# Kernel optimization log

Hardware: AMD Instinct MI355X
Metric: run time of the kernel (lower is better)

The kernel has to match this reference:

```python
import jax, jax.numpy as jnp
import numpy as np

L, D, DC, T, FF = 512, 512, 256, 128, 2048
P_COEF = 0.5


def layernorm(x, g, b):
    m = jnp.mean(x, axis=-1, keepdims=True)
    v = jnp.mean((x - m) ** 2, axis=-1, keepdims=True)
    return (x - m) / jnp.sqrt(v + 1e-5) * g + b


def conv_pool(t, w):
    # t: (L, N, D); torch attention_pool: permute -> (N, L, D), Conv1d over channels=L, length=D
    x = jnp.transpose(t, (1, 0, 2))  # (N, L, D)
    y = jax.lax.conv_general_dilated(x, w, window_strides=(2,), padding=[(1, 1)],
                                     dimension_numbers=("NCH", "OIH", "NCH"))
    return jnp.transpose(y, (1, 0, 2))  # (L, N, D//2)


def attn_fused(q, k):
    # q: (L, 1, d), k: (M, 1, d); faithful to module.attention with N=1 (squeeze(1))
    q2, k2 = q[:, 0], k[:, 0]
    scale = 1.0 / jnp.sqrt(jnp.asarray(q2.shape[1], q2.dtype))
    a = jax.nn.softmax((q2 @ k2.T) * scale, axis=-1)
    return (a @ k2 + q2)[:, None, :]  # fused residual add of q


def setup_inputs() -> dict:
    key = jax.random.key(0)
    ks = jax.random.split(key, 8)
    x = jax.random.normal(ks[0], (L, 1, D), jnp.float32)
    cached_k = jax.random.normal(ks[1], (T, L, 1, DC), jnp.float32)
    mem_mask = jax.random.randint(ks[2], (T,), 0, 2, jnp.int32)
    return {
        "x": x,
        "cached_k": cached_k,
        "ln1_g": jnp.ones((D,), jnp.float32),
        "ln1_b": jnp.zeros((D,), jnp.float32),
        "ln2_g": jnp.ones((D,), jnp.float32),
        "ln2_b": jnp.zeros((D,), jnp.float32),
        "w_compress_k": jax.random.normal(ks[3], (L, L, 3), jnp.float32) * (1.0 / np.sqrt(3 * L)),
        "w_compress_cur": jax.random.normal(ks[4], (L, L, 3), jnp.float32) * (1.0 / np.sqrt(3 * L)),
        "ap_w": jax.random.normal(ks[5], (DC, D), jnp.float32) * (1.0 / np.sqrt(DC)),
        "ap_b": jnp.zeros((D,), jnp.float32),
        "fc_w": jax.random.normal(ks[6], (D, FF), jnp.float32) * (1.0 / np.sqrt(D)),
        "fc_b": jnp.zeros((FF,), jnp.float32),
        "proj_w": jax.random.normal(ks[7], (FF, D), jnp.float32) * (1.0 / np.sqrt(FF)),
        "proj_b": jnp.zeros((D,), jnp.float32),
        "mem_mask": mem_mask,
    }


def reference(x, cached_k, ln1_g, ln1_b, ln2_g, ln2_b, w_compress_k, w_compress_cur,
              ap_w, ap_b, fc_w, fc_b, proj_w, proj_b, mem_mask):
    x1 = layernorm(x, ln1_g, ln1_b)                      # ln_1; q = k = x1
    # mask_memory: zero cached entries whose video name differs (per-entry, N=1)
    mem = cached_k * mem_mask.astype(x.dtype)[:, None, None, None]  # (T, L, 1, DC)
    k_cur = conv_pool(x1, w_compress_cur)                # (L, 1, DC) compress current k
    k = jnp.concatenate([mem.reshape(-1, 1, DC), k_cur], axis=0)    # ((T+1)*L, 1, DC)
    q = conv_pool(x1, w_compress_k)                      # k.shape[2]==256 branch: compress q
    selfatten = attn_fused(q, q)
    atten = attn_fused(q, k) + selfatten * P_COEF
    atten = atten @ ap_w + ap_b                          # attenproj 256 -> 512
    x2 = x1 + atten
    h = layernorm(x2, ln2_g, ln2_b)
    h = h @ fc_w + fc_b
    h = h * jax.nn.sigmoid(1.702 * h)                    # QuickGELU
    h = h @ proj_w + proj_b
    return x2 + h
```

## Files before the change

kernel.cpp:

```cpp
#include <hip/hip_runtime.h>
#include <hip/hip_bf16.h>

typedef unsigned short u16;
typedef unsigned int u32;
typedef __attribute__((ext_vector_type(8))) short bf16x8;
typedef __attribute__((ext_vector_type(4))) short bf16x4;
typedef __attribute__((ext_vector_type(4))) float f32x4;
typedef __attribute__((ext_vector_type(8))) u16 u16x8;
typedef __attribute__((ext_vector_type(4))) u16 u16x4;
typedef __attribute__((ext_vector_type(4))) u32 u32x4;

__device__ __forceinline__ u16 f2bf(float x){
  __hip_bfloat16 h = __float2bfloat16(x);
  return __builtin_bit_cast(u16, h);
}
__device__ __forceinline__ float bf2f(u16 u){
  __hip_bfloat16 h = __builtin_bit_cast(__hip_bfloat16, u);
  return __bfloat162float(h);
}

template<bool BF>
__global__ __launch_bounds__(256) void ln_kernel(const float* __restrict__ in,
    const float* __restrict__ g, const float* __restrict__ b,
    float* __restrict__ outf, u16* __restrict__ outb)
{
  int row = blockIdx.x, tid = threadIdx.x;
  const float* p = in + (size_t)row*512 + tid*2;
  float v0 = p[0], v1 = p[1];
  float s = v0+v1, ss = v0*v0+v1*v1;
  #pragma unroll
  for (int o=1;o<64;o<<=1){ s += __shfl_xor(s,o); ss += __shfl_xor(ss,o); }
  __shared__ float rs[4], rss[4];
  if ((tid&63)==0){ rs[tid>>6]=s; rss[tid>>6]=ss; }
  __syncthreads();
  s = rs[0]+rs[1]+rs[2]+rs[3]; ss = rss[0]+rss[1]+rss[2]+rss[3];
  float mean = s*(1.f/512.f);
  float var  = ss*(1.f/512.f) - mean*mean;
  float rstd = 1.f/sqrtf(var + 1e-5f);
  int d = tid*2;
  float o0 = (v0-mean)*rstd*g[d]   + b[d];
  float o1 = (v1-mean)*rstd*g[d+1] + b[d+1];
  if (BF){
    outb[(size_t)row*512+d]   = f2bf(o0);
    outb[(size_t)row*512+d+1] = f2bf(o1);
  } else {
    outf[(size_t)row*512+d]   = o0;
    outf[(size_t)row*512+d+1] = o1;
  }
}

__global__ __launch_bounds__(256) void xgT_kernel(const float* __restrict__ x1, u16* __restrict__ xgT)
{
  int h = blockIdx.x, tid = threadIdx.x;
  #pragma unroll
  for (int rep=0;rep<6;rep++){
    int k = rep*256 + tid;
    int i = k/3, kk = k - i*3;
    int pos = 2*h - 1 + kk;
    float v = (pos >= 0 && pos < 512) ? x1[(size_t)i*512 + pos] : 0.f;
    xgT[(size_t)h*1536 + k] = f2bf(v);
  }
}

__device__ __forceinline__ void transcvt_body(float (*t)[33],
    const float* __restrict__ in, u16* __restrict__ out, int K, int N, int bx, int by)
{
  int nb = bx*32, kb = by*32;
  int tx = threadIdx.x & 31, ty = threadIdx.x >> 5;
  #pragma unroll
  for (int i=0;i<32;i+=8) t[ty+i][tx] = in[(size_t)(kb+ty+i)*N + nb+tx];
  __syncthreads();
  #pragma unroll
  for (int i=0;i<32;i+=8) out[(size_t)(nb+ty+i)*K + kb+tx] = f2bf(t[tx][ty+i]);
}

__global__ __launch_bounds__(256) void prep_kernel(
    const float* __restrict__ x, const float* __restrict__ ln1g, const float* __restrict__ ln1b,
    const float* __restrict__ wk, const float* __restrict__ wc,
    const float* __restrict__ apw, const float* __restrict__ fcw, const float* __restrict__ pjw,
    const float* __restrict__ ck, const int* __restrict__ mask,
    float* __restrict__ x1,
    u16* __restrict__ wkcb, u16* __restrict__ apT, u16* __restrict__ fcT,
    u16* __restrict__ pjT, u16* __restrict__ kbf)
{
  __shared__ float t[32][33];
  __shared__ float rs[4], rss[4];
  int b = blockIdx.x, tid = threadIdx.x;
  if (b < 512){
    const float* p = x + (size_t)b*512 + tid*2;
    float v0 = p[0], v1 = p[1];
    float s = v0+v1, ss = v0*v0+v1*v1;
    #pragma unroll
    for (int o=1;o<64;o<<=1){ s += __shfl_xor(s,o); ss += __shfl_xor(ss,o); }
    if ((tid&63)==0){ rs[tid>>6]=s; rss[tid>>6]=ss; }
    __syncthreads();
    s = rs[0]+rs[1]+rs[2]+rs[3]; ss = rss[0]+rss[1]+rss[2]+rss[3];
    float mean = s*(1.f/512.f);
    float var  = ss*(1.f/512.f) - mean*mean;
    float rstd = 1.f/sqrtf(var + 1e-5f);
    int d = tid*2;
    x1[(size_t)b*512+d]   = (v0-mean)*rstd*ln1g[d]   + ln1b[d];
    x1[(size_t)b*512+d+1] = (v1-mean)*rstd*ln1g[d+1] + ln1b[d+1];
  } else if (b < 8704){
    int flat = (b-512)*256 + tid;
    int row = flat >> 5, seg = flat & 31;
    if (mask[row>>9] == 0) return;
    const float* src = ck + (size_t)row*256 + seg*8;
    u16x8 o;
    #pragma unroll
    for (int j=0;j<8;j++) o[j] = f2bf(src[j]);
    *(u16x8*)(kbf + (size_t)row*256 + seg*8) = o;
  } else if (b < 9472){
    size_t i = (size_t)((b-8704)*256 + tid)*8;
    const size_t half = (size_t)512*1536;
    const float* src = (i < half) ? (wk + i) : (wc + (i - half));
    u16x8 o;
    #pragma unroll
    for (int j=0;j<8;j++) o[j] = f2bf(src[j]);
    *(u16x8*)(wkcb + i) = o;
  } else if (b < 9600){
    int f = b - 9472;
    transcvt_body(t, apw, apT, 256, 512, f & 15, f >> 4);
  } else if (b < 10624){
    int f = b - 9600;
    transcvt_body(t, fcw, fcT, 512, 2048, f & 63, f >> 6);
  } else {
    int f = b - 10624;
    transcvt_body(t, pjw, pjT, 2048, 512, f & 15, f >> 4);
  }
}

template<int ACT, bool WF32, bool WBF, int W>
__global__ __launch_bounds__(64*W) void gemm4(
    const u16* __restrict__ A, const u16* __restrict__ B,
    const float* __restrict__ bias, const float* __restrict__ resid,
    float* __restrict__ outF, u16* __restrict__ outB, u16* __restrict__ outB2,
    int rowSplit, int M, int N, int K)
{
  __shared__ float red[W][32][33];
  int tid = threadIdx.x;
  int w = tid >> 6, lane = tid & 63;
  int lq = lane & 15, lg = lane >> 4;
  int m0 = blockIdx.y*32, n0 = blockIdx.x*32;
  int Ks = K / W;
  int kbeg = w * Ks;
  f32x4 acc00={0,0,0,0}, acc01={0,0,0,0}, acc10={0,0,0,0}, acc11={0,0,0,0};
  const u16* pa0 = A + (size_t)(m0+lq)*K + kbeg + lg*8;
  const u16* pa1 = pa0 + (size_t)16*K;
  const u16* pb0 = B + (size_t)(n0+lq)*K + kbeg + lg*8;
  const u16* pb1 = pb0 + (size_t)16*K;
  #pragma unroll 2
  for (int k0=0;k0<Ks;k0+=32){
    bf16x8 a0 = *(const bf16x8*)(pa0+k0);
    bf16x8 a1 = *(const bf16x8*)(pa1+k0);
    bf16x8 b0 = *(const bf16x8*)(pb0+k0);
    bf16x8 b1 = *(const bf16x8*)(pb1+k0);
    acc00 = __builtin_amdgcn_mfma_f32_16x16x32_bf16(a0,b0,acc00,0,0,0);
    acc01 = __builtin_amdgcn_mfma_f32_16x16x32_bf16(a0,b1,acc01,0,0,0);
    acc10 = __builtin_amdgcn_mfma_f32_16x16x32_bf16(a1,b0,acc10,0,0,0);
    acc11 = __builtin_amdgcn_mfma_f32_16x16x32_bf16(a1,b1,acc11,0,0,0);
  }
  f32x4 accs[2][2] = {{acc00,acc01},{acc10,acc11}};
  #pragma unroll
  for (int mi=0;mi<2;mi++)
    #pragma unroll
    for (int ni=0;ni<2;ni++)
      #pragma unroll
      for (int r=0;r<4;r++)
        red[w][mi*16+lg*4+r][ni*16+lq] = accs[mi][ni][r];
  __syncthreads();
  #pragma unroll
  for (int rr=0;rr<16/W;rr++){
    int cell = rr*64*W + tid;
    int row = cell >> 5, col = cell & 31;
    float v = 0.f;
    #pragma unroll
    for (int ww=0;ww<W;ww++) v += red[ww][row][col];
    int grow = m0 + row, gcol = n0 + col;
    if (bias)  v += bias[gcol];
    if (ACT==1) v = v/(1.f+__expf(-1.702f*v));
    if (resid) v += resid[(size_t)grow*N+gcol];
    if (WF32) outF[(size_t)grow*N+gcol] = v;
    if (WBF){
      if (grow < rowSplit) outB[(size_t)grow*N+gcol] = f2bf(v);
      else                 outB2[(size_t)(grow-rowSplit)*N+gcol] = f2bf(v);
    }
  }
}

__global__ __launch_bounds__(128) void attn_flash(
    const u16* __restrict__ qb, const u16* __restrict__ keys,
    const int* __restrict__ mask,
    u16* __restrict__ pO, float* __restrict__ pL)
{
  __shared__ u16 kv[2][8192];
  int tid = threadIdx.x;
  int w = tid >> 6, lane = tid & 63, lq = lane & 15, lg = lane >> 4;
  int bid = blockIdx.x;
  int c = ((bid >> 7) << 3) | (bid & 7);
  int qt = (bid >> 3) & 15;
  if (c >= 66) return;
  const u16* kp = keys;
  int kstart = c * 1024, off = 0, nt = 32;
  if (c == 65) { kp = qb; kstart = 0; nt = 16; }
  else if (c == 64) { kstart = 65536; nt = 16; }
  else {
    int m0 = mask[2*c], m1 = mask[2*c+1];
    if (!m0 && !m1) return;
    off = m0 ? 0 : 512;
    nt = ((m0 && m1) ? 32 : 16);
  }
  int qbase = qt*32 + w*16;

  bf16x8 qf[8];
  {
    const u16* qrow = qb + (size_t)(qbase+lq)*256 + lg*8;
    #pragma unroll
    for (int s=0;s<8;s++) qf[s] = *(const bf16x8*)(qrow + s*32);
  }
  f32x4 o[16];
  #pragma unroll
  for (int i=0;i<16;i++) o[i] = (f32x4){0,0,0,0};
  float l_acc = 0.f;

  auto kv3 = (__attribute__((address_space(3))) char*)&kv[0][0];
  unsigned kvaddr0 = (unsigned)(unsigned long long)kv3;
  const char* gbase = (const char*)kp + (size_t)(kstart+off)*512;

  #define STAGE(i, b) { \
    const char* tb = gbase + (size_t)(i)*16384; \
    _Pragma("unroll") \
    for (int rep=0; rep<8; rep++){ \
      int slot = rep*128 + tid; \
      int goff = ((slot&63)>>1)*512 + ((slot>>6)*16 + (slot&1)*8)*2; \
      __builtin_amdgcn_global_load_lds( \
        (const __attribute__((address_space(1))) unsigned*)(tb + goff), \
        (__attribute__((address_space(3))) unsigned*)(kv3 + (b)*16384 + (rep*128 + (tid & ~63))*16), \
        16, 0, 0); \
    } }

  #define ISSUE8(T, ab) \
    asm volatile( \
      "ds_read_b64_tr_b16 %0, %8 offset:0\n\t" \
      "ds_read_b64_tr_b16 %1, %8 offset:512\n\t" \
      "ds_read_b64_tr_b16 %2, %8 offset:1024\n\t" \
      "ds_read_b64_tr_b16 %3, %8 offset:1536\n\t" \
      "ds_read_b64_tr_b16 %4, %8 offset:2048\n\t" \
      "ds_read_b64_tr_b16 %5, %8 offset:2560\n\t" \
      "ds_read_b64_tr_b16 %6, %8 offset:3072\n\t" \
      "ds_read_b64_tr_b16 %7, %8 offset:3584\n\t" \
      : "=&v"(T[0]),"=&v"(T[1]),"=&v"(T[2]),"=&v"(T[3]), \
        "=&v"(T[4]),"=&v"(T[5]),"=&v"(T[6]),"=&v"(T[7]) \
      : "v"(ab) : "memory")

  #define MFMA4(T, base) { \
    bf16x8 v0_ = __builtin_shufflevector(T[0],T[1],0,1,2,3,4,5,6,7); \
    bf16x8 v1_ = __builtin_shufflevector(T[2],T[3],0,1,2,3,4,5,6,7); \
    bf16x8 v2_ = __builtin_shufflevector(T[4],T[5],0,1,2,3,4,5,6,7); \
    bf16x8 v3_ = __builtin_shufflevector(T[6],T[7],0,1,2,3,4,5,6,7); \
    o[(base)+0] = __builtin_amdgcn_mfma_f32_16x16x32_bf16(pa, v0_, o[(base)+0], 0,0,0); \
    o[(base)+1] = __builtin_amdgcn_mfma_f32_16x16x32_bf16(pa, v1_, o[(base)+1], 0,0,0); \
    o[(base)+2] = __builtin_amdgcn_mfma_f32_16x16x32_bf16(pa, v2_, o[(base)+2], 0,0,0); \
    o[(base)+3] = __builtin_amdgcn_mfma_f32_16x16x32_bf16(pa, v3_, o[(base)+3], 0,0,0); \
  }

  STAGE(0, 0);
  for (int i=0; i<nt; i++){
    int cur = i & 1;
    if (i+1 < nt){
      STAGE(i+1, cur^1);
      asm volatile("s_waitcnt vmcnt(8)" ::: "memory");
    } else {
      asm volatile("s_waitcnt vmcnt(0)" ::: "memory");
    }
    __syncthreads();

    const u16* kb = &kv[cur][0];
    f32x4 s0 = {0,0,0,0}, s1 = {0,0,0,0};
    #pragma unroll
    for (int s=0;s<8;s++){
      int e = (2*s + (lg>>1))*512 + lq*16 + (lg&1)*8;
      bf16x8 ka0 = *(const bf16x8*)(kb + e);
      bf16x8 ka1 = *(const bf16x8*)(kb + e + 256);
      s0 = __builtin_amdgcn_mfma_f32_16x16x32_bf16(ka0, qf[s], s0, 0,0,0);
      s1 = __builtin_amdgcn_mfma_f32_16x16x32_bf16(ka1, qf[s], s1, 0,0,0);
    }
    asm volatile("s_waitcnt lgkmcnt(0)" ::: "memory");

    unsigned trb = kvaddr0 + cur*16384 + lane*8;
    bf16x4 tA[8], tB[8], tC[8], tD[8];
    ISSUE8(tA, trb);
    ISSUE8(tB, trb + 4096);

    float p[8];
    #pragma unroll
    for (int r=0;r<4;r++){ p[r]   = __expf(s0[r]*0.0625f);
                           p[4+r] = __expf(s1[r]*0.0625f); }
    l_acc += (p[0]+p[1])+(p[2]+p[3])+((p[4]+p[5])+(p[6]+p[7]));
    u32 w0 = (u32)f2bf(p[0]) | ((u32)f2bf(p[1])<<16);
    u32 w1 = (u32)f2bf(p[2]) | ((u32)f2bf(p[3])<<16);
    u32 w2 = (u32)f2bf(p[4]) | ((u32)f2bf(p[5])<<16);
    u32 w3 = (u32)f2bf(p[6]) | ((u32)f2bf(p[7])<<16);
    u32x4 fq = {w0,w1,w2,w3};
    bf16x8 pa = __builtin_bit_cast(bf16x8, fq);

    asm volatile("s_waitcnt lgkmcnt(8)" ::: "memory");
    __builtin_amdgcn_sched_barrier(0);
    MFMA4(tA, 0);
    ISSUE8(tC, trb + 8192);
    asm volatile("s_waitcnt lgkmcnt(8)" ::: "memory");
    __builtin_amdgcn_sched_barrier(0);
    MFMA4(tB, 4);
    ISSUE8(tD, trb + 12288);
    asm volatile("s_waitcnt lgkmcnt(8)" ::: "memory");
    __builtin_amdgcn_sched_barrier(0);
    MFMA4(tC, 8);
    asm volatile("s_waitcnt lgkmcnt(0)" ::: "memory");
    __builtin_amdgcn_sched_barrier(0);
    MFMA4(tD, 12);
    __syncthreads();
  }
  #undef STAGE
  #undef ISSUE8
  #undef MFMA4

  l_acc += __shfl_xor(l_acc, 16);
  l_acc += __shfl_xor(l_acc, 32);
  size_t qrow = (size_t)c*512 + qbase;
  if (lane < 16) pL[qrow + lq] = l_acc;
  #pragma unroll
  for (int dt=0; dt<16; dt++){
    #pragma unroll
    for (int r=0;r<4;r++){
      pO[(qrow + lg*4 + r)*256 + dt*16 + lq] = f2bf(o[dt][r]);
    }
  }
}

__global__ __launch_bounds__(256) void attn_reduce(
    const u16* __restrict__ pO, const float* __restrict__ pL,
    const int* __restrict__ mask, const u16* __restrict__ qb,
    u16* __restrict__ attn_out)
{
  __shared__ f32x4 redO[4][64];
  __shared__ float redL[4];
  __shared__ float scnt[2];
  int q = blockIdx.x, tid = threadIdx.x;
  int cg = tid >> 6, dq = tid & 63;

  float mz = (tid < 128) ? ((mask[tid]==0) ? 1.f : 0.f) : 0.f;
  #pragma unroll
  for (int o=1;o<64;o<<=1) mz += __shfl_xor(mz, o);
  if ((tid&63)==0 && tid < 128) scnt[tid>>6] = mz;

  f32x4 acc = {0,0,0,0};
  float lsum = 0.f;
  for (int c = cg; c < 65; c += 4){
    bool valid = (c==64) || mask[2*c] || mask[2*c+1];
    if (!valid) continue;
    u16x4 v = *(const u16x4*)(pO + ((size_t)c*512+q)*256 + dq*4);
    acc[0] += bf2f(v[0]); acc[1] += bf2f(v[1]);
    acc[2] += bf2f(v[2]); acc[3] += bf2f(v[3]);
    if (dq==0) lsum += pL[(size_t)c*512+q];
  }
  redO[cg][dq] = acc;
  if (dq==0) redL[cg] = lsum;
  __syncthreads();
  if (tid < 64){
    f32x4 s = redO[0][tid];
    f32x4 s1 = redO[1][tid], s2 = redO[2][tid], s3 = redO[3][tid];
    s[0]+=s1[0]+s2[0]+s3[0]; s[1]+=s1[1]+s2[1]+s3[1];
    s[2]+=s1[2]+s2[2]+s3[2]; s[3]+=s1[3]+s2[3]+s3[3];
    float den = redL[0]+redL[1]+redL[2]+redL[3] + 512.f*(scnt[0]+scnt[1]);
    float ls  = pL[(size_t)65*512 + q];
    u16x4 sv = *(const u16x4*)(pO + ((size_t)65*512+q)*256 + tid*4);
    u16x4 qv = *(const u16x4*)(qb + (size_t)q*256 + tid*4);
    u16x4 ov;
    #pragma unroll
    for (int j=0;j<4;j++)
      ov[j] = f2bf(s[j]/den + 0.5f*bf2f(sv[j])/ls + 1.5f*bf2f(qv[j]));
    *(u16x4*)(attn_out + (size_t)q*256 + tid*4) = ov;
  }
}

extern "C" void kernel_launch(void* const* d_in, const int* in_sizes, int n_in,
                              void* d_out, int out_size, void* d_ws, size_t ws_size,
                              hipStream_t stream)
{
  const float* x    = (const float*)d_in[0];
  const float* ck   = (const float*)d_in[1];
  const float* ln1g = (const float*)d_in[2];
  const float* ln1b = (const float*)d_in[3];
  const float* ln2g = (const float*)d_in[4];
  const float* ln2b = (const float*)d_in[5];
  const float* wk   = (const float*)d_in[6];
  const float* wc   = (const float*)d_in[7];
  const float* apw  = (const float*)d_in[8];
  const float* apb  = (const float*)d_in[9];
  const float* fcw  = (const float*)d_in[10];
  const float* fcb  = (const float*)d_in[11];
  const float* pjw  = (const float*)d_in[12];
  const float* pjb  = (const float*)d_in[13];
  const int*   mask = (const int*)d_in[14];
  float* out = (float*)d_out;

  char* wsb = (char*)d_ws;
  float* x1    = (float*)(wsb + 0);
  float* x2    = (float*)(wsb + 1048576);
  u16*   aoutb = (u16*)  (wsb + 2097152);
  u16*   x2nb  = (u16*)  (wsb + 2359296);
  u16*   xgT   = (u16*)  (wsb + 2883584);
  u16*   apT   = (u16*)  (wsb + 3670016);
  u16*   fcT   = (u16*)  (wsb + 3932160);
  u16*   pjT   = (u16*)  (wsb + 6029312);
  u16*   qbf   = (u16*)  (wsb + 8126464);
  u16*   kbf   = (u16*)  (wsb + 8388608);
  float* pL    = (float*)(wsb + 42205184);
  u16*   pO    = (u16*)  (wsb + 42340352);
  u16*   wkcb  = (u16*)  (wsb + 42340352);
  u16*   hb    = (u16*)  (wsb + 42340352);

  prep_kernel<<<11648,256,0,stream>>>(x, ln1g, ln1b, wk, wc, apw, fcw, pjw, ck, mask,
      x1, wkcb, apT, fcT, pjT, kbf);
  xgT_kernel<<<256,256,0,stream>>>(x1, xgT);

  gemm4<0,false,true,8><<<dim3(8,32),512,0,stream>>>(wkcb, xgT, nullptr, nullptr,
      nullptr, qbf, kbf + (size_t)65536*256, 512, 1024, 256, 1536);

  attn_flash<<<1152,128,0,stream>>>(qbf, kbf, mask, pO, pL);
  attn_reduce<<<512,256,0,stream>>>(pO, pL, mask, qbf, aoutb);

  gemm4<0,true,false,4><<<dim3(16,16),256,0,stream>>>(aoutb, apT, apb, x1,
      x2, nullptr, nullptr, 512, 512, 512, 256);
  ln_kernel<true><<<512,256,0,stream>>>(x2, ln2g, ln2b, nullptr, x2nb);
  gemm4<1,false,true,4><<<dim3(64,16),256,0,stream>>>(x2nb, fcT, fcb, nullptr,
      nullptr, hb, hb, 4096, 512, 2048, 512);
  gemm4<0,true,false,8><<<dim3(16,16),512,0,stream>>>(hb, pjT, pjb, x2,
      out, nullptr, nullptr, 512, 512, 512, 2048);
}
```

Baseline: 114.9 us.

## Process two 16-row query tiles per wave in attention kernel to reuse K/V loads

Each wave now handles 32 query rows instead of 16, so every K tile staged in LDS and every transposed V read feeds twice as many MFMAs. The grid is halved to 576 blocks. This cuts global-to-LDS traffic and LDS reads per unit of compute, at the cost of doubled accumulator registers (lower occupancy) and fewer blocks in flight. The transposed-read pipelining was also simplified to a wait-all per group, which may expose more LDS latency.

```diff
diff --git a/kernel.cpp b/kernel.cpp
--- a/kernel.cpp
+++ b/kernel.cpp
@@ -197,8 +197,8 @@
   int tid = threadIdx.x;
   int w = tid >> 6, lane = tid & 63, lq = lane & 15, lg = lane >> 4;
   int bid = blockIdx.x;
-  int c = ((bid >> 7) << 3) | (bid & 7);
-  int qt = (bid >> 3) & 15;
+  int c = ((bid >> 6) << 3) | (bid & 7);
+  int qt = (bid >> 3) & 7;
   if (c >= 66) return;
   const u16* kp = keys;
   int kstart = c * 1024, off = 0, nt = 32;
@@ -210,18 +210,22 @@
     off = m0 ? 0 : 512;
     nt = ((m0 && m1) ? 32 : 16);
   }
-  int qbase = qt*32 + w*16;
-
-  bf16x8 qf[8];
+  int qbase = qt*64 + w*32;
+
+  bf16x8 qf0[8], qf1[8];
   {
-    const u16* qrow = qb + (size_t)(qbase+lq)*256 + lg*8;
-    #pragma unroll
-    for (int s=0;s<8;s++) qf[s] = *(const bf16x8*)(qrow + s*32);
-  }
-  f32x4 o[16];
-  #pragma unroll
-  for (int i=0;i<16;i++) o[i] = (f32x4){0,0,0,0};
-  float l_acc = 0.f;
+    const u16* qrowA = qb + (size_t)(qbase+lq)*256 + lg*8;
+    const u16* qrowB = qrowA + 16*256;
+    #pragma unroll
+    for (int s=0;s<8;s++){
+      qf0[s] = *(const bf16x8*)(qrowA + s*32);
+      qf1[s] = *(const bf16x8*)(qrowB + s*32);
+    }
+  }
+  f32x4 o0[16], o1[16];
+  #pragma unroll
+  for (int i=0;i<16;i++){ o0[i]=(f32x4){0,0,0,0}; o1[i]=(f32x4){0,0,0,0}; }
+  float l_accA = 0.f, l_accB = 0.f;
 
   auto kv3 = (__attribute__((address_space(3))) char*)&kv[0][0];
   unsigned kvaddr0 = (unsigned)(unsigned long long)kv3;
@@ -253,15 +257,19 @@
         "=&v"(T[4]),"=&v"(T[5]),"=&v"(T[6]),"=&v"(T[7]) \
       : "v"(ab) : "memory")
 
-  #define MFMA4(T, base) { \
+  #define MFMA8(T, base) { \
     bf16x8 v0_ = __builtin_shufflevector(T[0],T[1],0,1,2,3,4,5,6,7); \
     bf16x8 v1_ = __builtin_shufflevector(T[2],T[3],0,1,2,3,4,5,6,7); \
     bf16x8 v2_ = __builtin_shufflevector(T[4],T[5],0,1,2,3,4,5,6,7); \
     bf16x8 v3_ = __builtin_shufflevector(T[6],T[7],0,1,2,3,4,5,6,7); \
-    o[(base)+0] = __builtin_amdgcn_mfma_f32_16x16x32_bf16(pa, v0_, o[(base)+0], 0,0,0); \
-    o[(base)+1] = __builtin_amdgcn_mfma_f32_16x16x32_bf16(pa, v1_, o[(base)+1], 0,0,0); \
-    o[(base)+2] = __builtin_amdgcn_mfma_f32_16x16x32_bf16(pa, v2_, o[(base)+2], 0,0,0); \
-    o[(base)+3] = __builtin_amdgcn_mfma_f32_16x16x32_bf16(pa, v3_, o[(base)+3], 0,0,0); \
+    o0[(base)+0] = __builtin_amdgcn_mfma_f32_16x16x32_bf16(pa0, v0_, o0[(base)+0], 0,0,0); \
+    o1[(base)+0] = __builtin_amdgcn_mfma_f32_16x16x32_bf16(pa1, v0_, o1[(base)+0], 0,0,0); \
+    o0[(base)+1] = __builtin_amdgcn_mfma_f32_16x16x32_bf16(pa0, v1_, o0[(base)+1], 0,0,0); \
+    o1[(base)+1] = __builtin_amdgcn_mfma_f32_16x16x32_bf16(pa1, v1_, o1[(base)+1], 0,0,0); \
+    o0[(base)+2] = __builtin_amdgcn_mfma_f32_16x16x32_bf16(pa0, v2_, o0[(base)+2], 0,0,0); \
+    o1[(base)+2] = __builtin_amdgcn_mfma_f32_16x16x32_bf16(pa1, v2_, o1[(base)+2], 0,0,0); \
+    o0[(base)+3] = __builtin_amdgcn_mfma_f32_16x16x32_bf16(pa0, v3_, o0[(base)+3], 0,0,0); \
+    o1[(base)+3] = __builtin_amdgcn_mfma_f32_16x16x32_bf16(pa1, v3_, o1[(base)+3], 0,0,0); \
   }
 
   STAGE(0, 0);
@@ -276,63 +284,72 @@
     __syncthreads();
 
     const u16* kb = &kv[cur][0];
-    f32x4 s0 = {0,0,0,0}, s1 = {0,0,0,0};
+    f32x4 s0a={0,0,0,0}, s1a={0,0,0,0}, s0b={0,0,0,0}, s1b={0,0,0,0};
     #pragma unroll
     for (int s=0;s<8;s++){
       int e = (2*s + (lg>>1))*512 + lq*16 + (lg&1)*8;
       bf16x8 ka0 = *(const bf16x8*)(kb + e);
       bf16x8 ka1 = *(const bf16x8*)(kb + e + 256);
-      s0 = __builtin_amdgcn_mfma_f32_16x16x32_bf16(ka0, qf[s], s0, 0,0,0);
-      s1 = __builtin_amdgcn_mfma_f32_16x16x32_bf16(ka1, qf[s], s1, 0,0,0);
-    }
-    asm volatile("s_waitcnt lgkmcnt(0)" ::: "memory");
-
-    unsigned trb = kvaddr0 + cur*16384 + lane*8;
-    bf16x4 tA[8], tB[8], tC[8], tD[8];
-    ISSUE8(tA, trb);
-    ISSUE8(tB, trb + 4096);
-
-    float p[8];
-    #pragma unroll
-    for (int r=0;r<4;r++){ p[r]   = __expf(s0[r]*0.0625f);
-                           p[4+r] = __expf(s1[r]*0.0625f); }
-    l_acc += (p[0]+p[1])+(p[2]+p[3])+((p[4]+p[5])+(p[6]+p[7]));
-    u32 w0 = (u32)f2bf(p[0]) | ((u32)f2bf(p[1])<<16);
-    u32 w1 = (u32)f2bf(p[2]) | ((u32)f2bf(p[3])<<16);
-    u32 w2 = (u32)f2bf(p[4]) | ((u32)f2bf(p[5])<<16);
-    u32 w3 = (u32)f2bf(p[6]) | ((u32)f2bf(p[7])<<16);
-    u32x4 fq = {w0,w1,w2,w3};
-    bf16x8 pa = __builtin_bit_cast(bf16x8, fq);
-
-    asm volatile("s_waitcnt lgkmcnt(8)" ::: "memory");
-    __builtin_amdgcn_sched_barrier(0);
-    MFMA4(tA, 0);
-    ISSUE8(tC, trb + 8192);
-    asm volatile("s_waitcnt lgkmcnt(8)" ::: "memory");
-    __builtin_amdgcn_sched_barrier(0);
-    MFMA4(tB, 4);
-    ISSUE8(tD, trb + 12288);
-    asm volatile("s_waitcnt lgkmcnt(8)" ::: "memory");
-    __builtin_amdgcn_sched_barrier(0);
-    MFMA4(tC, 8);
+      s0a = __builtin_amdgcn_mfma_f32_16x16x32_bf16(ka0, qf0[s], s0a, 0,0,0);
+      s1a = __builtin_amdgcn_mfma_f32_16x16x32_bf16(ka1, qf0[s], s1a, 0,0,0);
+      s0b = __builtin_amdgcn_mfma_f32_16x16x32_bf16(ka0, qf1[s], s0b, 0,0,0);
+      s1b = __builtin_amdgcn_mfma_f32_16x16x32_bf16(ka1, qf1[s], s1b, 0,0,0);
+    }
     asm volatile("s_waitcnt lgkmcnt(0)" ::: "memory");
     __builtin_amdgcn_sched_barrier(0);
-    MFMA4(tD, 12);
+
+    bf16x8 pa0, pa1;
+    {
+      float p0=__expf(s0a[0]*0.0625f), p1=__expf(s0a[1]*0.0625f);
+      float p2=__expf(s0a[2]*0.0625f), p3=__expf(s0a[3]*0.0625f);
+      float p4=__expf(s1a[0]*0.0625f), p5=__expf(s1a[1]*0.0625f);
+      float p6=__expf(s1a[2]*0.0625f), p7=__expf(s1a[3]*0.0625f);
+      l_accA += (p0+p1)+(p2+p3)+((p4+p5)+(p6+p7));
+      u32x4 fq = { (u32)f2bf(p0)|((u32)f2bf(p1)<<16), (u32)f2bf(p2)|((u32)f2bf(p3)<<16),
+                   (u32)f2bf(p4)|((u32)f2bf(p5)<<16), (u32)f2bf(p6)|((u32)f2bf(p7)<<16) };
+      pa0 = __builtin_bit_cast(bf16x8, fq);
+    }
+    {
+      float p0=__expf(s0b[0]*0.0625f), p1=__expf(s0b[1]*0.0625f);
+      float p2=__expf(s0b[2]*0.0625f), p3=__expf(s0b[3]*0.0625f);
+      float p4=__expf(s1b[0]*0.0625f), p5=__expf(s1b[1]*0.0625f);
+      float p6=__expf(s1b[2]*0.0625f), p7=__expf(s1b[3]*0.0625f);
+      l_accB += (p0+p1)+(p2+p3)+((p4+p5)+(p6+p7));
+      u32x4 fq = { (u32)f2bf(p0)|((u32)f2bf(p1)<<16), (u32)f2bf(p2)|((u32)f2bf(p3)<<16),
+                   (u32)f2bf(p4)|((u32)f2bf(p5)<<16), (u32)f2bf(p6)|((u32)f2bf(p7)<<16) };
+      pa1 = __builtin_bit_cast(bf16x8, fq);
+    }
+
+    unsigned trb = kvaddr0 + cur*16384 + lane*8;
+    #pragma unroll
+    for (int g2=0; g2<4; g2++){
+      bf16x4 tt[8];
+      ISSUE8(tt, trb + g2*4096);
+      asm volatile("s_waitcnt lgkmcnt(0)" ::: "memory");
+      __builtin_amdgcn_sched_barrier(0);
+      MFMA8(tt, g2*4);
+    }
     __syncthreads();
   }
   #undef STAGE
   #undef ISSUE8
-  #undef MFMA4
-
-  l_acc += __shfl_xor(l_acc, 16);
-  l_acc += __shfl_xor(l_acc, 32);
+  #undef MFMA8
+
+  l_accA += __shfl_xor(l_accA, 16);
+  l_accA += __shfl_xor(l_accA, 32);
+  l_accB += __shfl_xor(l_accB, 16);
+  l_accB += __shfl_xor(l_accB, 32);
   size_t qrow = (size_t)c*512 + qbase;
-  if (lane < 16) pL[qrow + lq] = l_acc;
+  if (lane < 16){
+    pL[qrow + lq]      = l_accA;
+    pL[qrow + 16 + lq] = l_accB;
+  }
   #pragma unroll
   for (int dt=0; dt<16; dt++){
     #pragma unroll
     for (int r=0;r<4;r++){
-      pO[(qrow + lg*4 + r)*256 + dt*16 + lq] = f2bf(o[dt][r]);
+      pO[(qrow + lg*4 + r)*256 + dt*16 + lq]      = f2bf(o0[dt][r]);
+      pO[(qrow + 16 + lg*4 + r)*256 + dt*16 + lq] = f2bf(o1[dt][r]);
     }
   }
 }
@@ -427,7 +444,7 @@
   gemm4<0,false,true,8><<<dim3(8,32),512,0,stream>>>(wkcb, xgT, nullptr, nullptr,
       nullptr, qbf, kbf + (size_t)65536*256, 512, 1024, 256, 1536);
 
-  attn_flash<<<1152,128,0,stream>>>(qbf, kbf, mask, pO, pL);
+  attn_flash<<<576,128,0,stream>>>(qbf, kbf, mask, pO, pL);
   attn_reduce<<<512,256,0,stream>>>(pO, pL, mask, qbf, aoutb);
 
   gemm4<0,true,false,4><<<dim3(16,16),256,0,stream>>>(aoutb, apT, apb, x1,
```

Measured after the change: 124.2 us. 1.08x slower.
